# Kernel optimization log

Hardware: AMD Instinct MI355X
Metric: run time of the kernel (lower is better)

Reference implementation:

```python
import jax, jax.numpy as jnp
import numpy as np
import math

EPS = 1e-5
K = 4        # conv kernel size
N = 16       # d_state


def setup_inputs() -> dict:
    key = jax.random.key(0)
    b, l, d = 1, 2048, 1024
    di = 2 * d                      # inner channels after split
    dt_rank = math.ceil(d / 16)     # 64
    ks = jax.random.split(key, 8)
    s = 0.02
    return {
        "x": jax.random.normal(ks[0], (b, l, d), jnp.float32),
        "norm_scale": jnp.ones((d,), jnp.float32),
        "w_in": jax.random.normal(ks[1], (d, 4 * d), jnp.float32) * s,
        "conv_w": jax.random.normal(ks[2], (K, 1, di), jnp.float32) * 0.2,
        "conv_b": jnp.zeros((di,), jnp.float32),
        "A_log": jax.random.normal(ks[3], (di, N), jnp.float32) * 0.5,
        "D": jax.random.normal(ks[4], (di,), jnp.float32) * 0.1,
        "w_xproj": jax.random.normal(ks[5], (di, dt_rank + 2 * N), jnp.float32) * s,
        "w_dt": jax.random.normal(ks[6], (dt_rank, di), jnp.float32) * s,
        "b_dt": jnp.zeros((di,), jnp.float32),
        "w_out": jax.random.normal(ks[7], (di, d), jnp.float32) * s,
    }


def _causal_depthwise_conv(x, w, b):
    # x: (b,l,c), w: (K,1,c). Original pads (K-1,K-1) then slices [:, :l] == causal left-pad.
    c = x.shape[-1]
    y = jax.lax.conv_general_dilated(
        x, w, window_strides=(1,), padding=[(K - 1, 0)],
        dimension_numbers=("NWC", "WIO", "NWC"), feature_group_count=c)
    return y + b


def reference(x, norm_scale, w_in, conv_w, conv_b, A_log, D, w_xproj, w_dt, b_dt, w_out):
    dt_rank = w_dt.shape[0]
    # RMSNorm (mean=False, bias=False), scale only
    h = x * jax.lax.rsqrt(jnp.mean(x * x, axis=-1, keepdims=True) + EPS) * norm_scale
    h = h @ w_in                         # (b,l,4d)
    xs, res = jnp.split(h, 2, axis=-1)   # each (b,l,2d)
    res = jax.nn.silu(res)
    xs = jax.nn.silu(_causal_depthwise_conv(xs, conv_w, conv_b))
    proj = xs @ w_xproj                  # (b,l,dt_rank+2N)
    delta, B, C = jnp.split(proj, [dt_rank, dt_rank + N], axis=-1)
    delta = jax.nn.softplus(delta @ w_dt + b_dt)          # (b,l,c)
    A = -jnp.exp(A_log)                                   # (c,n)
    deltaA = jnp.exp(delta[..., None] * A)                # (b,l,c,n)
    deltaBx = (delta * xs)[..., None] * B[:, :, None, :]  # (b,l,c,n)

    def combine(e_i, e_j):
        a_i, b_i = e_i
        a_j, b_j = e_j
        return (a_i * a_j, a_j * b_i + b_j)

    _, ys = jax.lax.associative_scan(combine, (deltaA, deltaBx), axis=1)
    y = jnp.einsum("blcn,bln->blc", ys, C)
    out = (y + xs * D) * res
    return x + out @ w_out
```

## Files before the change

### kernel.cpp

```cpp
#include <hip/hip_runtime.h>

typedef short short8 __attribute__((ext_vector_type(8)));
typedef float floatx4 __attribute__((ext_vector_type(4)));
typedef unsigned int u32;

__device__ __forceinline__ float b2f(unsigned short u) {
    union { unsigned int i; float f; } v; v.i = ((unsigned int)u) << 16; return v.f;
}
__device__ __forceinline__ float hi2f(u32 p) {
    union { unsigned int i; float f; } v; v.i = p & 0xFFFF0000u; return v.f;
}
__device__ __forceinline__ float lo2f(u32 p) {
    union { unsigned int i; float f; } v; v.i = p << 16; return v.f;
}
__device__ __forceinline__ unsigned short f2b(float f) {
    union { unsigned int i; float f; } v; v.f = f;
    unsigned int r = v.i + 0x7FFFu + ((v.i >> 16) & 1u);
    return (unsigned short)(r >> 16);
}
__device__ __forceinline__ float ld(const void* p, size_t i, int f) {
    return f ? ((const float*)p)[i] : b2f(((const unsigned short*)p)[i]);
}
__device__ __forceinline__ int dtf(const void* scale) {
    return (((const unsigned short*)scale)[0] == 0x3F80u) ? 0 : 1;
}
__device__ __forceinline__ void gload16(const unsigned short* g, unsigned short* l) {
    __builtin_amdgcn_global_load_lds(
        (const __attribute__((address_space(1))) u32*)(const void*)g,
        (__attribute__((address_space(3))) u32*)(void*)l, 16, 0, 0);
}
template<int CTRL>
__device__ __forceinline__ float dpp_add(float y) {
    union { float f; int i; } u, r;
    u.f = y;
    r.i = __builtin_amdgcn_update_dpp(0, u.i, CTRL, 0xF, 0xF, true);
    return y + r.f;
}

__global__ __launch_bounds__(256) void prep_kernel(
    const void* x, const void* scale, unsigned short* __restrict__ h,
    const void* w_in, unsigned short* __restrict__ wT,
    const void* w_out, unsigned short* __restrict__ woT)
{
    const int f = dtf(scale);
    const int b = blockIdx.x, tid = threadIdx.x;
    if (b < 2048) {
        const int t = b;
        float xv[4];
        float ss = 0.f;
        #pragma unroll
        for (int j = 0; j < 4; j++) {
            xv[j] = ld(x, (size_t)t * 1024 + j * 256 + tid, f);
            ss += xv[j] * xv[j];
        }
        #pragma unroll
        for (int o = 32; o > 0; o >>= 1) ss += __shfl_down(ss, o);
        __shared__ float sr[4];
        if ((tid & 63) == 0) sr[tid >> 6] = ss;
        __syncthreads();
        float r = rsqrtf((sr[0] + sr[1] + sr[2] + sr[3]) * (1.f / 1024.f) + 1e-5f);
        #pragma unroll
        for (int j = 0; j < 4; j++) {
            int i = j * 256 + tid;
            h[(size_t)t * 1024 + i] = f2b(xv[j] * r * ld(scale, i, f));
        }
    } else if (b < 3072) {
        __shared__ unsigned short tile[64][68];
        const int idx = b - 2048;
        const int n0 = (idx & 63) * 64, k0 = (idx >> 6) * 64;
        #pragma unroll
        for (int j = 0; j < 16; j++) {
            int ii = tid + 256 * j, r = ii >> 6, c = ii & 63;
            tile[r][c] = f2b(ld(w_in, (size_t)(k0 + r) * 4096 + n0 + c, f));
        }
        __syncthreads();
        #pragma unroll
        for (int j = 0; j < 16; j++) {
            int ii = tid + 256 * j, r = ii >> 6, c = ii & 63;
            wT[(size_t)(n0 + r) * 1024 + k0 + c] = tile[c][r];
        }
    } else {
        __shared__ unsigned short tile[64][68];
        const int idx = b - 3072;
        const int n0 = (idx & 15) * 64, k0 = (idx >> 4) * 64;
        #pragma unroll
        for (int j = 0; j < 16; j++) {
            int ii = tid + 256 * j, r = ii >> 6, c = ii & 63;
            tile[r][c] = f2b(ld(w_out, (size_t)(k0 + r) * 1024 + n0 + c, f));
        }
        __syncthreads();
        #pragma unroll
        for (int j = 0; j < 16; j++) {
            int ii = tid + 256 * j, r = ii >> 6, c = ii & 63;
            woT[(size_t)(n0 + r) * 2048 + k0 + c] = tile[c][r];
        }
    }
}

template<int KDIM, int NDIM, int TM, int MODE>
__global__ __launch_bounds__(256) void gemm_bt_kernel(
    const unsigned short* __restrict__ A, const unsigned short* __restrict__ BT,
    void* out0, unsigned short* out1, const void* xres, const void* nscale)
{
    constexpr int RT = TM / 32;
    const int f = dtf(nscale);
    __shared__ __align__(16) unsigned short As[TM * 64];
    __shared__ __align__(16) unsigned short Bs[64 * 64];
    const int t = threadIdx.x, w = t >> 6, lane = t & 63;
    const int q = lane >> 4, low = lane & 15;
    const int row0 = blockIdx.y * TM, n0 = blockIdx.x * 64;
    const int wy = w >> 1, wx = w & 1;

    floatx4 acc[RT][2];
    #pragma unroll
    for (int i = 0; i < RT; i++)
        #pragma unroll
        for (int j = 0; j < 2; j++) acc[i][j] = (floatx4){0.f, 0.f, 0.f, 0.f};

    const int srow = lane >> 3, scol = (lane & 7) * 8;
    const unsigned short* a_src = A + (size_t)(row0 + w * (TM / 4) + srow) * KDIM + scol;
    const unsigned short* b_src = BT + (size_t)(n0 + w * 16 + srow) * KDIM + scol;

    for (int k0 = 0; k0 < KDIM; k0 += 64) {
        #pragma unroll
        for (int i = 0; i < TM / 32; i++)
            gload16(a_src + k0 + i * 8 * KDIM, &As[(w * (TM / 4) + i * 8) * 64]);
        #pragma unroll
        for (int i = 0; i < 2; i++)
            gload16(b_src + k0 + i * 8 * KDIM, &Bs[(w * 16 + i * 8) * 64]);
        __syncthreads();
        #pragma unroll
        for (int kh = 0; kh < 2; kh++) {
            short8 af[RT];
            #pragma unroll
            for (int rt = 0; rt < RT; rt++)
                af[rt] = *(const short8*)&As[(wy * (TM / 2) + rt * 16 + low) * 64 + kh * 32 + q * 8];
            #pragma unroll
            for (int nt = 0; nt < 2; nt++) {
                short8 bf = *(const short8*)&Bs[(wx * 32 + nt * 16 + low) * 64 + kh * 32 + q * 8];
                #pragma unroll
                for (int rt = 0; rt < RT; rt++)
                    acc[rt][nt] = __builtin_amdgcn_mfma_f32_16x16x32_bf16(af[rt], bf, acc[rt][nt], 0, 0, 0);
            }
        }
        __syncthreads();
    }

    #pragma unroll
    for (int nt = 0; nt < 2; nt++) {
        const int col = n0 + wx * 32 + nt * 16 + low;
        #pragma unroll
        for (int rt = 0; rt < RT; rt++) {
            #pragma unroll
            for (int r = 0; r < 4; r++) {
                const int row = row0 + wy * (TM / 2) + rt * 16 + q * 4 + r;
                float v = acc[rt][nt][r];
                if (MODE == 0) {
                    if (col < NDIM / 2) {
                        ((unsigned short*)out0)[(size_t)row * (NDIM / 2) + col] = f2b(v);
                    } else {
                        float s = v / (1.f + __expf(-v));
                        out1[(size_t)row * (NDIM / 2) + (col - NDIM / 2)] = f2b(s);
                    }
                } else {
                    size_t idx = (size_t)row * NDIM + col;
                    float o = v + ld(xres, idx, f);
                    if (f) ((float*)out0)[idx] = o;
                    else   ((unsigned short*)out0)[idx] = f2b(o);
                }
            }
        }
    }
}

__global__ __launch_bounds__(256) void conv_kernel(
    const unsigned short* __restrict__ xs_raw, const void* conv_w,
    const void* conv_b, unsigned short* __restrict__ xs_conv, const void* nscale)
{
    const int f = dtf(nscale);
    int id = blockIdx.x * 256 + threadIdx.x;
    int t = id >> 8, c8 = (id & 255) * 8;
    float acc[8];
    if (f) {
        const float* bf = (const float*)conv_b + c8;
        float4 b0 = *(const float4*)bf, b1 = *(const float4*)(bf + 4);
        acc[0] = b0.x; acc[1] = b0.y; acc[2] = b0.z; acc[3] = b0.w;
        acc[4] = b1.x; acc[5] = b1.y; acc[6] = b1.z; acc[7] = b1.w;
    } else {
        uint4 bv = *(const uint4*)((const unsigned short*)conv_b + c8);
        const unsigned short* bp = (const unsigned short*)&bv;
        #pragma unroll
        for (int j = 0; j < 8; j++) acc[j] = b2f(bp[j]);
    }
    #pragma unroll
    for (int k = 0; k < 4; k++) {
        int tt = t - 3 + k;
        if (tt >= 0) {
            uint4 xv = *(const uint4*)(xs_raw + (size_t)tt * 2048 + c8);
            const unsigned short* xp = (const unsigned short*)&xv;
            float wv[8];
            if (f) {
                const float* wf = (const float*)conv_w + (size_t)k * 2048 + c8;
                float4 w0 = *(const float4*)wf, w1 = *(const float4*)(wf + 4);
                wv[0] = w0.x; wv[1] = w0.y; wv[2] = w0.z; wv[3] = w0.w;
                wv[4] = w1.x; wv[5] = w1.y; wv[6] = w1.z; wv[7] = w1.w;
            } else {
                uint4 wu = *(const uint4*)((const unsigned short*)conv_w + (size_t)k * 2048 + c8);
                const unsigned short* wp = (const unsigned short*)&wu;
                #pragma unroll
                for (int j = 0; j < 8; j++) wv[j] = b2f(wp[j]);
            }
            #pragma unroll
            for (int j = 0; j < 8; j++) acc[j] += wv[j] * b2f(xp[j]);
        }
    }
    unsigned short outv[8];
    #pragma unroll
    for (int j = 0; j < 8; j++) {
        float s = acc[j] / (1.f + __expf(-acc[j]));
        outv[j] = f2b(s);
    }
    *(uint4*)(xs_conv + (size_t)t * 2048 + c8) = *(const uint4*)outv;
}

__global__ __launch_bounds__(256) void xproj_gemm_kernel(
    const unsigned short* __restrict__ A, const void* B,
    float* __restrict__ partials, const void* nscale)
{
    const int f = dtf(nscale);
    __shared__ __align__(16) unsigned short As[64 * 32];
    __shared__ __align__(16) unsigned short Bs[64 * 32];
    const int t = threadIdx.x;
    const int row0 = blockIdx.y * 64, n0 = blockIdx.x * 64;
    const int ks = blockIdx.z;
    const int wave = t >> 6, lane = t & 63;
    const int q = lane >> 4, low = lane & 15;
    floatx4 acc[4];
    #pragma unroll
    for (int i = 0; i < 4; i++) acc[i] = (floatx4){0.f, 0.f, 0.f, 0.f};
    const int ar = t >> 2, ac = (t & 3) * 8;
    const int bk = t >> 3, bn = (t & 7) * 8;
    const int col0 = n0 + bn;
    const int kbeg = ks * 256, kend = kbeg + 256;
    for (int k0 = kbeg; k0 < kend; k0 += 32) {
        uint4 av = *(const uint4*)(A + (size_t)(row0 + ar) * 2048 + k0 + ac);
        *(uint4*)&As[ar * 32 + ac] = av;
        unsigned short bu[8];
        if (col0 < 96) {
            if (f) {
                const float* Bf = (const float*)B + (size_t)(k0 + bk) * 96 + col0;
                float4 b0 = *(const float4*)Bf, b1 = *(const float4*)(Bf + 4);
                bu[0] = f2b(b0.x); bu[1] = f2b(b0.y); bu[2] = f2b(b0.z); bu[3] = f2b(b0.w);
                bu[4] = f2b(b1.x); bu[5] = f2b(b1.y); bu[6] = f2b(b1.z); bu[7] = f2b(b1.w);
            } else {
                uint4 bv = *(const uint4*)((const unsigned short*)B + (size_t)(k0 + bk) * 96 + col0);
                *(uint4*)bu = bv;
            }
        } else {
            #pragma unroll
            for (int j = 0; j < 8; j++) bu[j] = 0;
        }
        #pragma unroll
        for (int j = 0; j < 8; j++) Bs[(bn + j) * 32 + bk] = bu[j];
        __syncthreads();
        short8 af = *(const short8*)&As[(wave * 16 + low) * 32 + q * 8];
        #pragma unroll
        for (int i = 0; i < 4; i++) {
            short8 bfr = *(const short8*)&Bs[(i * 16 + low) * 32 + q * 8];
            acc[i] = __builtin_amdgcn_mfma_f32_16x16x32_bf16(af, bfr, acc[i], 0, 0, 0);
        }
        __syncthreads();
    }
    float* out = partials + (size_t)ks * (2048 * 128);
    #pragma unroll
    for (int i = 0; i < 4; i++) {
        int col = n0 + i * 16 + low;
        #pragma unroll
        for (int r = 0; r < 4; r++) {
            int row = row0 + wave * 16 + q * 4 + r;
            out[(size_t)row * 128 + col] = acc[i][r];
        }
    }
}

__global__ __launch_bounds__(256) void xproj_reduce_kernel(
    const float* __restrict__ partials, float* __restrict__ proj)
{
    int id = blockIdx.x * 256 + threadIdx.x;
    float s = 0.f;
    #pragma unroll
    for (int k = 0; k < 8; k++) s += partials[(size_t)k * (2048 * 128) + id];
    proj[id] = s;
}

__global__ __launch_bounds__(256) void delta_gemm_kernel(
    const float* __restrict__ proj, const void* B, const void* b_dt,
    unsigned short* __restrict__ delta, const void* nscale)
{
    const int f = dtf(nscale);
    __shared__ __align__(16) unsigned short As[64 * 32];
    __shared__ __align__(16) unsigned short Bs[64 * 32];
    const int t = threadIdx.x;
    const int row0 = blockIdx.y * 64, n0 = blockIdx.x * 64;
    const int wave = t >> 6, lane = t & 63;
    const int q = lane >> 4, low = lane & 15;
    floatx4 acc[4];
    #pragma unroll
    for (int i = 0; i < 4; i++) acc[i] = (floatx4){0.f, 0.f, 0.f, 0.f};
    const int ar = t >> 2, ac = (t & 3) * 8;
    const int bk = t >> 3, bn = (t & 7) * 8;
    #pragma unroll
    for (int k0 = 0; k0 < 64; k0 += 32) {
        const float* Ap = proj + (size_t)(row0 + ar) * 128 + k0 + ac;
        float4 a0 = *(const float4*)Ap, a1 = *(const float4*)(Ap + 4);
        As[ar * 32 + ac + 0] = f2b(a0.x); As[ar * 32 + ac + 1] = f2b(a0.y);
        As[ar * 32 + ac + 2] = f2b(a0.z); As[ar * 32 + ac + 3] = f2b(a0.w);
        As[ar * 32 + ac + 4] = f2b(a1.x); As[ar * 32 + ac + 5] = f2b(a1.y);
        As[ar * 32 + ac + 6] = f2b(a1.z); As[ar * 32 + ac + 7] = f2b(a1.w);
        unsigned short bu[8];
        if (f) {
            const float* Bp = (const float*)B + (size_t)(k0 + bk) * 2048 + n0 + bn;
            float4 b0 = *(const float4*)Bp, b1 = *(const float4*)(Bp + 4);
            bu[0] = f2b(b0.x); bu[1] = f2b(b0.y); bu[2] = f2b(b0.z); bu[3] = f2b(b0.w);
            bu[4] = f2b(b1.x); bu[5] = f2b(b1.y); bu[6] = f2b(b1.z); bu[7] = f2b(b1.w);
        } else {
            uint4 bv = *(const uint4*)((const unsigned short*)B + (size_t)(k0 + bk) * 2048 + n0 + bn);
            const unsigned short* bp = (const unsigned short*)&bv;
            #pragma unroll
            for (int j = 0; j < 8; j++) bu[j] = bp[j];
        }
        #pragma unroll
        for (int j = 0; j < 8; j++) Bs[(bn + j) * 32 + bk] = bu[j];
        __syncthreads();
        short8 af = *(const short8*)&As[(wave * 16 + low) * 32 + q * 8];
        #pragma unroll
        for (int i = 0; i < 4; i++) {
            short8 bfr = *(const short8*)&Bs[(i * 16 + low) * 32 + q * 8];
            acc[i] = __builtin_amdgcn_mfma_f32_16x16x32_bf16(af, bfr, acc[i], 0, 0, 0);
        }
        __syncthreads();
    }
    #pragma unroll
    for (int i = 0; i < 4; i++) {
        int col = n0 + i * 16 + low;
        float bias = ld(b_dt, col, f);
        #pragma unroll
        for (int r = 0; r < 4; r++) {
            int row = row0 + wave * 16 + q * 4 + r;
            float v = acc[i][r] + bias;
            float sp = fmaxf(v, 0.f) + log1pf(__expf(-fabsf(v)));
            delta[(size_t)row * 2048 + col] = f2b(sp);
        }
    }
}

__global__ __launch_bounds__(256) void scanA_kernel(
    const unsigned short* __restrict__ delta, const unsigned short* __restrict__ xs,
    const float* __restrict__ proj, const void* A_log,
    float* __restrict__ Aprod, float* __restrict__ Send, const void* nscale)
{
    const int f = dtf(nscale);
    const int chunk = blockIdx.x, c0 = blockIdx.y * 16, t0 = chunk * 128;
    __shared__ __align__(16) u32 dxl[16 * 132];
    __shared__ __align__(16) float Bt[16 * 132];
    const int tid = threadIdx.x;
    #pragma unroll
    for (int j = 0; j < 4; j++) {
        int idx = tid + 256 * j;
        int t = idx >> 3, cp = (idx & 7) * 2;
        u32 dpair = *(const u32*)(delta + (size_t)(t0 + t) * 2048 + c0 + cp);
        u32 xpair = *(const u32*)(xs    + (size_t)(t0 + t) * 2048 + c0 + cp);
        dxl[cp * 132 + t]       = (dpair << 16) | (xpair & 0xFFFFu);
        dxl[(cp + 1) * 132 + t] = (dpair & 0xFFFF0000u) | (xpair >> 16);
    }
    #pragma unroll
    for (int j = 0; j < 8; j++) {
        int idx = tid + 256 * j;
        int t = idx >> 4, n = idx & 15;
        Bt[n * 132 + t] = proj[(size_t)(t0 + t) * 128 + 64 + n];
    }
    __syncthreads();
    const int cl = tid >> 4, n = tid & 15;
    const float A = -__expf(ld(A_log, (size_t)(c0 + cl) * 16 + n, f));
    float s = 0.f, ap = 1.f;
    for (int t4 = 0; t4 < 128; t4 += 4) {
        uint4  dx4 = *(const uint4*)&dxl[cl * 132 + t4];
        float4 b4  = *(const float4*)&Bt[n * 132 + t4];
        const u32* dxp = (const u32*)&dx4;
        const float* bp = (const float*)&b4;
        #pragma unroll
        for (int j = 0; j < 4; j++) {
            u32 p = dxp[j];
            float dv = hi2f(p), xv = lo2f(p);
            float a = __expf(dv * A);
            s = a * s + dv * xv * bp[j];
            ap *= a;
        }
    }
    size_t o = (size_t)chunk * 32768 + (size_t)c0 * 16 + tid;
    Aprod[o] = ap;
    Send[o]  = s;
}

__global__ __launch_bounds__(256) void scanC_kernel(
    const unsigned short* __restrict__ delta, const unsigned short* __restrict__ xs,
    const float* __restrict__ proj, const void* A_log, const void* Dv,
    const float* __restrict__ Aprod, const float* __restrict__ Send,
    const unsigned short* __restrict__ res, unsigned short* __restrict__ inner,
    const void* nscale)
{
    const int f = dtf(nscale);
    const int chunk = blockIdx.x, c0 = blockIdx.y * 16, t0 = chunk * 128;
    __shared__ __align__(16) u32 dxl[16 * 132];
    __shared__ __align__(16) float Bt[16 * 132];
    __shared__ __align__(16) float Ct[16 * 132];
    __shared__ __align__(16) float yl[16 * 132];
    __shared__ float Dl[16];
    const int tid = threadIdx.x;
    if (tid < 16) Dl[tid] = ld(Dv, c0 + tid, f);
    const int g = c0 * 16 + tid;
    float s = 0.f;
    for (int k = 0; k < chunk; k++)
        s = Aprod[(size_t)k * 32768 + g] * s + Send[(size_t)k * 32768 + g];
    #pragma unroll
    for (int j = 0; j < 4; j++) {
        int idx = tid + 256 * j;
        int t = idx >> 3, cp = (idx & 7) * 2;
        u32 dpair = *(const u32*)(delta + (size_t)(t0 + t) * 2048 + c0 + cp);
        u32 xpair = *(const u32*)(xs    + (size_t)(t0 + t) * 2048 + c0 + cp);
        dxl[cp * 132 + t]       = (dpair << 16) | (xpair & 0xFFFFu);
        dxl[(cp + 1) * 132 + t] = (dpair & 0xFFFF0000u) | (xpair >> 16);
    }
    #pragma unroll
    for (int j = 0; j < 8; j++) {
        int idx = tid + 256 * j;
        int t = idx >> 4, n = idx & 15;
        Bt[n * 132 + t] = proj[(size_t)(t0 + t) * 128 + 64 + n];
        Ct[n * 132 + t] = proj[(size_t)(t0 + t) * 128 + 80 + n];
    }
    __syncthreads();
    const int cl = tid >> 4, n = tid & 15;
    const float A = -__expf(ld(A_log, (size_t)(c0 + cl) * 16 + n, f));
    for (int t4 = 0; t4 < 128; t4 += 4) {
        uint4  dx4 = *(const uint4*)&dxl[cl * 132 + t4];
        float4 b4  = *(const float4*)&Bt[n * 132 + t4];
        float4 c4  = *(const float4*)&Ct[n * 132 + t4];
        const u32* dxp = (const u32*)&dx4;
        const float* bp = (const float*)&b4;
        const float* cp = (const float*)&c4;
        #pragma unroll
        for (int j = 0; j < 4; j++) {
            u32 p = dxp[j];
            float dv = hi2f(p), xv = lo2f(p);
            float a = __expf(dv * A);
            s = a * s + dv * xv * bp[j];
            float y = s * cp[j];
            y = dpp_add<0x111>(y);
            y = dpp_add<0x112>(y);
            y = dpp_add<0x114>(y);
            y = dpp_add<0x118>(y);
            if (n == 15) yl[cl * 132 + t4 + j] = y;
        }
    }
    __syncthreads();
    const int et = tid >> 1, ech = (tid & 1) * 8;
    size_t gbase = (size_t)(t0 + et) * 2048 + c0 + ech;
    uint4 rv4 = *(const uint4*)(res + gbase);
    const unsigned short* rp = (const unsigned short*)&rv4;
    unsigned short outv[8];
    #pragma unroll
    for (int j = 0; j < 8; j++) {
        int c = ech + j;
        float y  = yl[c * 132 + et];
        float xv = lo2f(dxl[c * 132 + et]);
        float o  = (y + xv * Dl[c]) * b2f(rp[j]);
        outv[j] = f2b(o);
    }
    *(uint4*)(inner + gbase) = *(const uint4*)outv;
}

extern "C" void kernel_launch(void* const* d_in, const int* in_sizes, int n_in,
                              void* d_out, int out_size, void* d_ws, size_t ws_size,
                              hipStream_t stream) {
    const void* x       = d_in[0];
    const void* nscale  = d_in[1];
    const void* w_in    = d_in[2];
    const void* conv_w  = d_in[3];
    const void* conv_b  = d_in[4];
    const void* A_log   = d_in[5];
    const void* Dv      = d_in[6];
    const void* w_xproj = d_in[7];
    const void* w_dt    = d_in[8];
    const void* b_dt    = d_in[9];
    const void* w_out   = d_in[10];

    char* ws = (char*)d_ws;
    const size_t MB = 1048576;
    unsigned short* xs_raw  = (unsigned short*)(ws);
    unsigned short* res_s   = (unsigned short*)(ws + 8 * MB);
    unsigned short* xs_conv = (unsigned short*)(ws + 16 * MB);
    unsigned short* delta   = (unsigned short*)(ws + 24 * MB);
    unsigned short* h_norm  = (unsigned short*)(ws + 32 * MB);
    unsigned short* wT      = (unsigned short*)(ws + 36 * MB);
    unsigned short* woT     = (unsigned short*)(ws + 44 * MB);
    float*          partials= (float*)(ws + 48 * MB);
    float*          proj    = (float*)(ws + 56 * MB);
    float*          Aprod   = (float*)(ws + 57 * MB);
    float*          Send    = (float*)(ws + 59 * MB);
    unsigned short* inner   = res_s;

    prep_kernel<<<3584, 256, 0, stream>>>(x, nscale, h_norm, w_in, wT, w_out, woT);
    gemm_bt_kernel<1024, 4096, 128, 0><<<dim3(64, 16), 256, 0, stream>>>(
        h_norm, wT, xs_raw, res_s, nullptr, nscale);
    conv_kernel<<<2048, 256, 0, stream>>>(xs_raw, conv_w, conv_b, xs_conv, nscale);
    xproj_gemm_kernel<<<dim3(2, 32, 8), 256, 0, stream>>>(xs_conv, w_xproj, partials, nscale);
    xproj_reduce_kernel<<<1024, 256, 0, stream>>>(partials, proj);
    delta_gemm_kernel<<<dim3(32, 32), 256, 0, stream>>>(proj, w_dt, b_dt, delta, nscale);
    scanA_kernel<<<dim3(16, 128), 256, 0, stream>>>(delta, xs_conv, proj, A_log, Aprod, Send, nscale);
    scanC_kernel<<<dim3(16, 128), 256, 0, stream>>>(delta, xs_conv, proj, A_log, Dv, Aprod, Send, res_s, inner, nscale);
    gemm_bt_kernel<2048, 1024, 64, 1><<<dim3(16, 32), 256, 0, stream>>>(
        inner, woT, d_out, nullptr, x, nscale);
}
```

Before: 270.6 us.

## Fuse two-pass chunked scan into single decoupled-lookback kernel with flags

Measured after the change: 459.6 us. 1.7x slower.

```diff
diff --git a/kernel.cpp b/kernel.cpp
--- a/kernel.cpp
+++ b/kernel.cpp
@@ -354,16 +354,28 @@
     }
 }
 
-__global__ __launch_bounds__(256) void scanA_kernel(
+__global__ __launch_bounds__(256) void scan_fused_kernel(
     const unsigned short* __restrict__ delta, const unsigned short* __restrict__ xs,
-    const float* __restrict__ proj, const void* A_log,
-    float* __restrict__ Aprod, float* __restrict__ Send, const void* nscale)
+    const float* __restrict__ proj, const void* A_log, const void* Dv,
+    float* __restrict__ stateBuf, unsigned int* __restrict__ flags,
+    unsigned int* __restrict__ vcnt,
+    const unsigned short* __restrict__ res, unsigned short* __restrict__ inner,
+    const void* nscale)
 {
     const int f = dtf(nscale);
-    const int chunk = blockIdx.x, c0 = blockIdx.y * 16, t0 = chunk * 128;
     __shared__ __align__(16) u32 dxl[16 * 132];
     __shared__ __align__(16) float Bt[16 * 132];
+    __shared__ __align__(16) float Ct[16 * 132];
+    __shared__ __align__(16) float yl[16 * 132];
+    __shared__ float Dl[16];
+    __shared__ unsigned int vbid_s;
     const int tid = threadIdx.x;
+    if (tid == 0) vbid_s = atomicAdd(vcnt, 1u);
+    __syncthreads();
+    const int vbid = (int)vbid_s;
+    const int chunk = vbid >> 7, cg = vbid & 127;
+    const int c0 = cg * 16, t0 = chunk * 128;
+    if (tid < 16) Dl[tid] = ld(Dv, c0 + tid, f);
     #pragma unroll
     for (int j = 0; j < 4; j++) {
         int idx = tid + 256 * j;
@@ -378,11 +390,12 @@
         int idx = tid + 256 * j;
         int t = idx >> 4, n = idx & 15;
         Bt[n * 132 + t] = proj[(size_t)(t0 + t) * 128 + 64 + n];
+        Ct[n * 132 + t] = proj[(size_t)(t0 + t) * 128 + 80 + n];
     }
     __syncthreads();
     const int cl = tid >> 4, n = tid & 15;
     const float A = -__expf(ld(A_log, (size_t)(c0 + cl) * 16 + n, f));
-    float s = 0.f, ap = 1.f;
+    float sl = 0.f, ap = 1.f;
     for (int t4 = 0; t4 < 128; t4 += 4) {
         uint4  dx4 = *(const uint4*)&dxl[cl * 132 + t4];
         float4 b4  = *(const float4*)&Bt[n * 132 + t4];
@@ -393,54 +406,31 @@
             u32 p = dxp[j];
             float dv = hi2f(p), xv = lo2f(p);
             float a = __expf(dv * A);
-            s = a * s + dv * xv * bp[j];
+            sl = a * sl + dv * xv * bp[j];
             ap *= a;
         }
     }
-    size_t o = (size_t)chunk * 32768 + (size_t)c0 * 16 + tid;
-    Aprod[o] = ap;
-    Send[o]  = s;
-}
-
-__global__ __launch_bounds__(256) void scanC_kernel(
-    const unsigned short* __restrict__ delta, const unsigned short* __restrict__ xs,
-    const float* __restrict__ proj, const void* A_log, const void* Dv,
-    const float* __restrict__ Aprod, const float* __restrict__ Send,
-    const unsigned short* __restrict__ res, unsigned short* __restrict__ inner,
-    const void* nscale)
-{
-    const int f = dtf(nscale);
-    const int chunk = blockIdx.x, c0 = blockIdx.y * 16, t0 = chunk * 128;
-    __shared__ __align__(16) u32 dxl[16 * 132];
-    __shared__ __align__(16) float Bt[16 * 132];
-    __shared__ __align__(16) float Ct[16 * 132];
-    __shared__ __align__(16) float yl[16 * 132];
-    __shared__ float Dl[16];
-    const int tid = threadIdx.x;
-    if (tid < 16) Dl[tid] = ld(Dv, c0 + tid, f);
     const int g = c0 * 16 + tid;
-    float s = 0.f;
-    for (int k = 0; k < chunk; k++)
-        s = Aprod[(size_t)k * 32768 + g] * s + Send[(size_t)k * 32768 + g];
-    #pragma unroll
-    for (int j = 0; j < 4; j++) {
-        int idx = tid + 256 * j;
-        int t = idx >> 3, cp = (idx & 7) * 2;
-        u32 dpair = *(const u32*)(delta + (size_t)(t0 + t) * 2048 + c0 + cp);
-        u32 xpair = *(const u32*)(xs    + (size_t)(t0 + t) * 2048 + c0 + cp);
-        dxl[cp * 132 + t]       = (dpair << 16) | (xpair & 0xFFFFu);
-        dxl[(cp + 1) * 132 + t] = (dpair & 0xFFFF0000u) | (xpair >> 16);
-    }
-    #pragma unroll
-    for (int j = 0; j < 8; j++) {
-        int idx = tid + 256 * j;
-        int t = idx >> 4, n = idx & 15;
-        Bt[n * 132 + t] = proj[(size_t)(t0 + t) * 128 + 64 + n];
-        Ct[n * 132 + t] = proj[(size_t)(t0 + t) * 128 + 80 + n];
-    }
-    __syncthreads();
-    const int cl = tid >> 4, n = tid & 15;
-    const float A = -__expf(ld(A_log, (size_t)(c0 + cl) * 16 + n, f));
+    float pred = 0.f;
+    if (chunk > 0) {
+        if (tid == 0) {
+            while (__hip_atomic_load(&flags[(chunk - 1) * 128 + cg],
+                    __ATOMIC_ACQUIRE, __HIP_MEMORY_SCOPE_AGENT) == 0u)
+                __builtin_amdgcn_s_sleep(1);
+        }
+        __syncthreads();
+        pred = __hip_atomic_load(&stateBuf[(size_t)(chunk - 1) * 32768 + g],
+                                 __ATOMIC_RELAXED, __HIP_MEMORY_SCOPE_AGENT);
+    }
+    if (chunk < 15) {
+        __hip_atomic_store(&stateBuf[(size_t)chunk * 32768 + g], ap * pred + sl,
+                           __ATOMIC_RELAXED, __HIP_MEMORY_SCOPE_AGENT);
+        __syncthreads();
+        if (tid == 0)
+            __hip_atomic_store(&flags[chunk * 128 + cg], 1u,
+                               __ATOMIC_RELEASE, __HIP_MEMORY_SCOPE_AGENT);
+    }
+    float s = pred;
     for (int t4 = 0; t4 < 128; t4 += 4) {
         uint4  dx4 = *(const uint4*)&dxl[cl * 132 + t4];
         float4 b4  = *(const float4*)&Bt[n * 132 + t4];
@@ -505,9 +495,12 @@
     unsigned short* woT     = (unsigned short*)(ws + 44 * MB);
     float*          partials= (float*)(ws + 48 * MB);
     float*          proj    = (float*)(ws + 56 * MB);
-    float*          Aprod   = (float*)(ws + 57 * MB);
-    float*          Send    = (float*)(ws + 59 * MB);
+    unsigned int*   flags   = (unsigned int*)(ws + 57 * MB);
+    unsigned int*   vcnt    = (unsigned int*)(ws + 57 * MB + 8192);
+    float*          stateBuf= (float*)(ws + 58 * MB);
     unsigned short* inner   = res_s;
+
+    hipMemsetAsync(ws + 57 * MB, 0, 16384, stream);
 
     prep_kernel<<<3584, 256, 0, stream>>>(x, nscale, h_norm, w_in, wT, w_out, woT);
     gemm_bt_kernel<1024, 4096, 128, 0><<<dim3(64, 16), 256, 0, stream>>>(
@@ -516,8 +509,8 @@
     xproj_gemm_kernel<<<dim3(2, 32, 8), 256, 0, stream>>>(xs_conv, w_xproj, partials, nscale);
     xproj_reduce_kernel<<<1024, 256, 0, stream>>>(partials, proj);
     delta_gemm_kernel<<<dim3(32, 32), 256, 0, stream>>>(proj, w_dt, b_dt, delta, nscale);
-    scanA_kernel<<<dim3(16, 128), 256, 0, stream>>>(delta, xs_conv, proj, A_log, Aprod, Send, nscale);
-    scanC_kernel<<<dim3(16, 128), 256, 0, stream>>>(delta, xs_conv, proj, A_log, Dv, Aprod, Send, res_s, inner, nscale);
+    scan_fused_kernel<<<2048, 256, 0, stream>>>(
+        delta, xs_conv, proj, A_log, Dv, stateBuf, flags, vcnt, res_s, inner, nscale);
     gemm_bt_kernel<2048, 1024, 64, 1><<<dim3(16, 32), 256, 0, stream>>>(
         inner, woT, d_out, nullptr, x, nscale);
 }
```
